# Kernel optimization log

Measured on AMD Instinct MI355X. Metric: run time of the kernel, lower is better.

Reference implementation:

```python
import jax, jax.numpy as jnp
import numpy as np

N = 100000
E = 1600000
IN_DIM = 64
HID = 64


def _glorot(key, shape):
    fan_in, fan_out = shape[0], shape[1]
    lim = np.sqrt(6.0 / (fan_in + fan_out))
    return jax.random.uniform(key, shape, jnp.float32, -lim, lim)


def setup_inputs() -> dict:
    key = jax.random.key(0)
    ks = jax.random.split(key, 14)
    x = jax.random.normal(ks[0], (N, IN_DIM), jnp.float32)
    edge_index = jax.random.randint(ks[1], (2, E), 0, N, jnp.int64)
    dims = [(IN_DIM, HID), (HID, HID), (HID, HID), (HID, 1)]
    inp = {"x": x, "edge_index": edge_index}
    for i, (di, do) in enumerate(dims, start=1):
        inp[f"Wself{i}"] = _glorot(ks[2 + 3 * (i - 1)], (di, do))
        inp[f"Wneigh{i}"] = _glorot(ks[3 + 3 * (i - 1)], (di, do))
        inp[f"b{i}"] = jnp.zeros((do,), jnp.float32)
    return inp


def _gn_block(h, src, dst, deg_inv, Wself, Wneigh, b, act):
    # gather -> scatter-add -> mean -> dense transform (GraphConv-style)
    msg = h[src]                                           # [E, d]
    agg = jax.ops.segment_sum(msg, dst, num_segments=N)    # [N, d]
    agg = agg * deg_inv                                    # mean aggregation
    out = h @ Wself + agg @ Wneigh + b
    return act(out)


def reference(x, edge_index, Wself1, Wneigh1, b1, Wself2, Wneigh2, b2,
              Wself3, Wneigh3, b3, Wself4, Wneigh4, b4):
    src, dst = edge_index[0], edge_index[1]
    deg = jax.ops.segment_sum(jnp.ones((E,), x.dtype), dst, num_segments=N)
    deg_inv = (1.0 / jnp.maximum(deg, 1.0))[:, None]       # [N, 1]
    relu = jax.nn.relu
    h = _gn_block(x, src, dst, deg_inv, Wself1, Wneigh1, b1, relu)
    h = _gn_block(h, src, dst, deg_inv, Wself2, Wneigh2, b2, relu)
    h = _gn_block(h, src, dst, deg_inv, Wself3, Wneigh3, b3, relu)
    h = _gn_block(h, src, dst, deg_inv, Wself4, Wneigh4, b4, lambda z: z)
    return jax.nn.sigmoid(h)                               # [N, 1]
```

## Files before the change

kernel.cpp:

```cpp
#include <hip/hip_runtime.h>
#include <hip/hip_bf16.h>
#include <math.h>


using bfrag = __attribute__((ext_vector_type(8))) short;
using ffrag = __attribute__((ext_vector_type(4))) float;

#define BKT_SHIFT 9
#define BKT_NODES (1 << BKT_SHIFT)

__device__ __forceinline__ int load_idx32(const int* __restrict__ ei32, int is64,
                                          long long pos) {
    return is64 ? ei32[2 * pos] : ei32[pos];
}

__device__ __forceinline__ unsigned short f2b_rne(float f) {
    union { float f; unsigned u; } c;
    c.f = f;
    unsigned r = c.u + 0x7FFFu + ((c.u >> 16) & 1u);
    return (unsigned short)(r >> 16);
}

__device__ __forceinline__ float b2f(unsigned short u) {
    union { unsigned u; float f; } c;
    c.u = ((unsigned)u) << 16;
    return c.f;
}

__global__ void bprep_init_kernel(
    const float* __restrict__ Ws1, const float* __restrict__ Wn1,
    const float* __restrict__ Ws2, const float* __restrict__ Wn2,
    const float* __restrict__ Ws3, const float* __restrict__ Wn3,
    unsigned short* __restrict__ bthi, unsigned short* __restrict__ btlo,
    const int* __restrict__ ei, int* __restrict__ bktc, int* __restrict__ flag) {
    if (blockIdx.x == 0) {
        bktc[threadIdx.x] = 0;
        if (threadIdx.x == 0) {
            int allz = 1;
            for (int i = 0; i < 32; ++i)
                if (ei[2 * i + 1] != 0) allz = 0;
            *flag = allz;
        }
    }
    int i = blockIdx.x * 256 + threadIdx.x;
    if (i >= 3 * 8192) return;
    int layer = i >> 13;
    int j = i & 8191;
    int n = j >> 7, k = j & 127;
    const float* Ws = layer == 0 ? Ws1 : (layer == 1 ? Ws2 : Ws3);
    const float* Wn = layer == 0 ? Wn1 : (layer == 1 ? Wn2 : Wn3);
    float v = (k < 64) ? Ws[k * 64 + n] : Wn[(k - 64) * 64 + n];
    unsigned short hi = f2b_rne(v);
    bthi[i] = hi;
    btlo[i] = f2b_rne(v - b2f(hi));
}

__global__ void split_x_kernel(const float4* __restrict__ in, ushort4* __restrict__ hi,
                               int n4) {
    int i = blockIdx.x * blockDim.x + threadIdx.x;
    if (i >= n4) return;
    float4 v = in[i];
    ushort4 h;
    h.x = f2b_rne(v.x); h.y = f2b_rne(v.y); h.z = f2b_rne(v.z); h.w = f2b_rne(v.w);
    hi[i] = h;
}

__global__ __launch_bounds__(256) void binA_kernel(
    const int* __restrict__ ei32, const int* __restrict__ flagp,
    int* __restrict__ bktCnt, unsigned* __restrict__ bins, int E, int nbkt,
    int cap, int chunksz) {
    __shared__ int cnt[256];
    __shared__ int base[256];
    int is64 = *flagp;
    int elo = blockIdx.x * chunksz;
    int ehi = min(E, elo + chunksz);
    if (elo >= E) return;
    for (int i = threadIdx.x; i < nbkt; i += 256) cnt[i] = 0;
    __syncthreads();
    for (int e = elo + (int)threadIdx.x; e < ehi; e += 256) {
        int dst = load_idx32(ei32, is64, (long long)E + e);
        atomicAdd(&cnt[dst >> BKT_SHIFT], 1);
    }
    __syncthreads();
    for (int i = threadIdx.x; i < nbkt; i += 256) {
        base[i] = atomicAdd(&bktCnt[i], cnt[i]);
        cnt[i] = 0;
    }
    __syncthreads();
    for (int e = elo + (int)threadIdx.x; e < ehi; e += 256) {
        int dst = load_idx32(ei32, is64, (long long)E + e);
        int src = load_idx32(ei32, is64, e);
        int b = dst >> BKT_SHIFT;
        int r = atomicAdd(&cnt[b], 1);
        bins[(size_t)b * cap + base[b] + r] =
            ((unsigned)(dst & (BKT_NODES - 1)) << 23) | (unsigned)src;
    }
}

__global__ __launch_bounds__(256) void bucketCSR_kernel(
    const int* __restrict__ bktCnt, const unsigned* __restrict__ bins,
    int* __restrict__ off, int* __restrict__ offe, int* __restrict__ col,
    float* __restrict__ dinv, int N, int cap) {
    __shared__ int deg[BKT_NODES];
    __shared__ int loc[BKT_NODES];
    __shared__ int ssum[256];
    int b = blockIdx.x;
    int lo = b << BKT_SHIFT;
    int n = min(BKT_NODES, N - lo);
    for (int i = threadIdx.x; i < BKT_NODES; i += 256) deg[i] = 0;
    __syncthreads();
    int cnt = bktCnt[b];
    const unsigned* bb = bins + (size_t)b * cap;
    for (int i = threadIdx.x; i < cnt; i += 256)
        atomicAdd(&deg[bb[i] >> 23], 1);
    __syncthreads();
    int t = threadIdx.x;
    int d0 = deg[2 * t], d1 = deg[2 * t + 1];
    int s = d0 + d1;
    ssum[t] = s;
    __syncthreads();
    for (int o = 1; o < 256; o <<= 1) {
        int v = (t >= o) ? ssum[t - o] : 0;
        __syncthreads();
        ssum[t] += v;
        __syncthreads();
    }
    int excl = ssum[t] - s;
    loc[2 * t] = excl;
    loc[2 * t + 1] = excl + d0;
    __syncthreads();
    int base = b * cap;
    for (int i = threadIdx.x; i < n; i += 256) {
        int d = deg[i];
        off[lo + i] = base + loc[i];
        offe[lo + i] = base + loc[i] + d;
        dinv[lo + i] = 1.0f / fmaxf((float)d, 1.0f);
    }
    __syncthreads();
    for (int i = threadIdx.x; i < cnt; i += 256) {
        unsigned p = bb[i];
        int pos = atomicAdd(&loc[p >> 23], 1);
        col[base + pos] = (int)(p & 0x7FFFFFu);
    }
}

#define AGG_STRIDE 72
__global__ __launch_bounds__(256) void layer_fused_kernel(
    const unsigned short* __restrict__ Hhi, const int* __restrict__ off,
    const int* __restrict__ offe, const int* __restrict__ col,
    const float* __restrict__ dinv,
    const unsigned short* __restrict__ Bthi, const unsigned short* __restrict__ Btlo,
    const float* __restrict__ b, unsigned short* __restrict__ Dhi, int N) {
    __shared__ unsigned short aggL[4 * 16 * AGG_STRIDE];
    int wave = threadIdx.x >> 6;
    int lane = threadIdx.x & 63;
    int g = lane >> 4;
    int t16 = lane & 15;
    int n0 = blockIdx.x * 64 + wave * 16;
    unsigned short* myAgg = aggL + wave * 16 * AGG_STRIDE;
    for (int i = 0; i < 16; ++i) {
        int n = n0 + i;
        if (n >= N) {
            if (g == 0) {
                ushort4 z = {0, 0, 0, 0};
                *(ushort4*)&myAgg[i * AGG_STRIDE + t16 * 4] = z;
            }
            continue;
        }
        int e = off[n], end = offe[n];
        float4 a0 = make_float4(0.f, 0.f, 0.f, 0.f);
        float4 a1 = make_float4(0.f, 0.f, 0.f, 0.f);
        float4 a2 = make_float4(0.f, 0.f, 0.f, 0.f);
        float4 a3 = make_float4(0.f, 0.f, 0.f, 0.f);
        for (; e + 16 <= end; e += 16) {
            int s0 = col[e + g];
            int s1 = col[e + 4 + g];
            int s2 = col[e + 8 + g];
            int s3 = col[e + 12 + g];
            ushort4 u0 = *(const ushort4*)&Hhi[(size_t)s0 * 64 + t16 * 4];
            ushort4 u1 = *(const ushort4*)&Hhi[(size_t)s1 * 64 + t16 * 4];
            ushort4 u2 = *(const ushort4*)&Hhi[(size_t)s2 * 64 + t16 * 4];
            ushort4 u3 = *(const ushort4*)&Hhi[(size_t)s3 * 64 + t16 * 4];
            a0.x += b2f(u0.x); a0.y += b2f(u0.y); a0.z += b2f(u0.z); a0.w += b2f(u0.w);
            a1.x += b2f(u1.x); a1.y += b2f(u1.y); a1.z += b2f(u1.z); a1.w += b2f(u1.w);
            a2.x += b2f(u2.x); a2.y += b2f(u2.y); a2.z += b2f(u2.z); a2.w += b2f(u2.w);
            a3.x += b2f(u3.x); a3.y += b2f(u3.y); a3.z += b2f(u3.z); a3.w += b2f(u3.w);
        }
        for (; e + 8 <= end; e += 8) {
            int s0 = col[e + g];
            int s1 = col[e + 4 + g];
            ushort4 u0 = *(const ushort4*)&Hhi[(size_t)s0 * 64 + t16 * 4];
            ushort4 u1 = *(const ushort4*)&Hhi[(size_t)s1 * 64 + t16 * 4];
            a0.x += b2f(u0.x); a0.y += b2f(u0.y); a0.z += b2f(u0.z); a0.w += b2f(u0.w);
            a1.x += b2f(u1.x); a1.y += b2f(u1.y); a1.z += b2f(u1.z); a1.w += b2f(u1.w);
        }
        for (; e < end; e += 4) {
            if (e + g < end) {
                int s0 = col[e + g];
                ushort4 u0 = *(const ushort4*)&Hhi[(size_t)s0 * 64 + t16 * 4];
                a2.x += b2f(u0.x); a2.y += b2f(u0.y); a2.z += b2f(u0.z); a2.w += b2f(u0.w);
            }
        }
        float4 acc;
        acc.x = (a0.x + a1.x) + (a2.x + a3.x);
        acc.y = (a0.y + a1.y) + (a2.y + a3.y);
        acc.z = (a0.z + a1.z) + (a2.z + a3.z);
        acc.w = (a0.w + a1.w) + (a2.w + a3.w);
#pragma unroll
        for (int msk = 16; msk <= 32; msk <<= 1) {
            acc.x += __shfl_xor(acc.x, msk, 64);
            acc.y += __shfl_xor(acc.y, msk, 64);
            acc.z += __shfl_xor(acc.z, msk, 64);
            acc.w += __shfl_xor(acc.w, msk, 64);
        }
        if (g == 0) {
            float di = dinv[n];
            ushort4 h;
            h.x = f2b_rne(acc.x * di);
            h.y = f2b_rne(acc.y * di);
            h.z = f2b_rne(acc.z * di);
            h.w = f2b_rne(acc.w * di);
            *(ushort4*)&myAgg[i * AGG_STRIDE + t16 * 4] = h;
        }
    }
    int m = t16, quad = g;
    int nr = n0 + m;
    if (nr > N - 1) nr = N - 1;
    const unsigned short* hrow = Hhi + (size_t)nr * 64 + quad * 8;
    bfrag ah[4];
    ah[0] = *(const bfrag*)(hrow);
    ah[1] = *(const bfrag*)(hrow + 32);
    ah[2] = *(const bfrag*)&myAgg[m * AGG_STRIDE + quad * 8];
    ah[3] = *(const bfrag*)&myAgg[m * AGG_STRIDE + 32 + quad * 8];
#pragma unroll
    for (int t = 0; t < 4; ++t) {
        float bl = b[t * 16 + m];
        ffrag acc = {bl, bl, bl, bl};
#pragma unroll
        for (int c = 0; c < 4; ++c) {
            bfrag bh = *(const bfrag*)(Bthi + (size_t)(t * 16 + m) * 128 + c * 32 + quad * 8);
            bfrag bw = *(const bfrag*)(Btlo + (size_t)(t * 16 + m) * 128 + c * 32 + quad * 8);
            acc = __builtin_amdgcn_mfma_f32_16x16x32_bf16(ah[c], bh, acc, 0, 0, 0);
            acc = __builtin_amdgcn_mfma_f32_16x16x32_bf16(ah[c], bw, acc, 0, 0, 0);
        }
#pragma unroll
        for (int r = 0; r < 4; ++r) {
            int node = n0 + quad * 4 + r;
            if (node < N)
                Dhi[(size_t)node * 64 + t * 16 + m] = f2b_rne(fmaxf(acc[r], 0.f));
        }
    }
}

__global__ __launch_bounds__(256) void layer_fused_last_kernel(
    const unsigned short* __restrict__ Hhi, const int* __restrict__ off,
    const int* __restrict__ offe, const int* __restrict__ col,
    const float* __restrict__ dinv,
    const unsigned short* __restrict__ Bthi, const unsigned short* __restrict__ Btlo,
    const float* __restrict__ b, const float* __restrict__ Ws4,
    const float* __restrict__ Wn4, float* __restrict__ sbuf,
    float* __restrict__ gbuf, int N) {
    __shared__ unsigned short aggL[4 * 16 * AGG_STRIDE];
    int wave = threadIdx.x >> 6;
    int lane = threadIdx.x & 63;
    int g = lane >> 4;
    int t16 = lane & 15;
    int n0 = blockIdx.x * 64 + wave * 16;
    unsigned short* myAgg = aggL + wave * 16 * AGG_STRIDE;
    for (int i = 0; i < 16; ++i) {
        int n = n0 + i;
        if (n >= N) {
            if (g == 0) {
                ushort4 z = {0, 0, 0, 0};
                *(ushort4*)&myAgg[i * AGG_STRIDE + t16 * 4] = z;
            }
            continue;
        }
        int e = off[n], end = offe[n];
        float4 a0 = make_float4(0.f, 0.f, 0.f, 0.f);
        float4 a1 = make_float4(0.f, 0.f, 0.f, 0.f);
        float4 a2 = make_float4(0.f, 0.f, 0.f, 0.f);
        float4 a3 = make_float4(0.f, 0.f, 0.f, 0.f);
        for (; e + 16 <= end; e += 16) {
            int s0 = col[e + g];
            int s1 = col[e + 4 + g];
            int s2 = col[e + 8 + g];
            int s3 = col[e + 12 + g];
            ushort4 u0 = *(const ushort4*)&Hhi[(size_t)s0 * 64 + t16 * 4];
            ushort4 u1 = *(const ushort4*)&Hhi[(size_t)s1 * 64 + t16 * 4];
            ushort4 u2 = *(const ushort4*)&Hhi[(size_t)s2 * 64 + t16 * 4];
            ushort4 u3 = *(const ushort4*)&Hhi[(size_t)s3 * 64 + t16 * 4];
            a0.x += b2f(u0.x); a0.y += b2f(u0.y); a0.z += b2f(u0.z); a0.w += b2f(u0.w);
            a1.x += b2f(u1.x); a1.y += b2f(u1.y); a1.z += b2f(u1.z); a1.w += b2f(u1.w);
            a2.x += b2f(u2.x); a2.y += b2f(u2.y); a2.z += b2f(u2.z); a2.w += b2f(u2.w);
            a3.x += b2f(u3.x); a3.y += b2f(u3.y); a3.z += b2f(u3.z); a3.w += b2f(u3.w);
        }
        for (; e + 8 <= end; e += 8) {
            int s0 = col[e + g];
            int s1 = col[e + 4 + g];
            ushort4 u0 = *(const ushort4*)&Hhi[(size_t)s0 * 64 + t16 * 4];
            ushort4 u1 = *(const ushort4*)&Hhi[(size_t)s1 * 64 + t16 * 4];
            a0.x += b2f(u0.x); a0.y += b2f(u0.y); a0.z += b2f(u0.z); a0.w += b2f(u0.w);
            a1.x += b2f(u1.x); a1.y += b2f(u1.y); a1.z += b2f(u1.z); a1.w += b2f(u1.w);
        }
        for (; e < end; e += 4) {
            if (e + g < end) {
                int s0 = col[e + g];
                ushort4 u0 = *(const ushort4*)&Hhi[(size_t)s0 * 64 + t16 * 4];
                a2.x += b2f(u0.x); a2.y += b2f(u0.y); a2.z += b2f(u0.z); a2.w += b2f(u0.w);
            }
        }
        float4 acc;
        acc.x = (a0.x + a1.x) + (a2.x + a3.x);
        acc.y = (a0.y + a1.y) + (a2.y + a3.y);
        acc.z = (a0.z + a1.z) + (a2.z + a3.z);
        acc.w = (a0.w + a1.w) + (a2.w + a3.w);
#pragma unroll
        for (int msk = 16; msk <= 32; msk <<= 1) {
            acc.x += __shfl_xor(acc.x, msk, 64);
            acc.y += __shfl_xor(acc.y, msk, 64);
            acc.z += __shfl_xor(acc.z, msk, 64);
            acc.w += __shfl_xor(acc.w, msk, 64);
        }
        if (g == 0) {
            float di = dinv[n];
            ushort4 h;
            h.x = f2b_rne(acc.x * di);
            h.y = f2b_rne(acc.y * di);
            h.z = f2b_rne(acc.z * di);
            h.w = f2b_rne(acc.w * di);
            *(ushort4*)&myAgg[i * AGG_STRIDE + t16 * 4] = h;
        }
    }
    int m = t16, quad = g;
    int nr = n0 + m;
    if (nr > N - 1) nr = N - 1;
    const unsigned short* hrow = Hhi + (size_t)nr * 64 + quad * 8;
    bfrag ah[4];
    ah[0] = *(const bfrag*)(hrow);
    ah[1] = *(const bfrag*)(hrow + 32);
    ah[2] = *(const bfrag*)&myAgg[m * AGG_STRIDE + quad * 8];
    ah[3] = *(const bfrag*)&myAgg[m * AGG_STRIDE + 32 + quad * 8];
    ffrag accs[4];
#pragma unroll
    for (int t = 0; t < 4; ++t) {
        float bl = b[t * 16 + m];
        ffrag acc = {bl, bl, bl, bl};
#pragma unroll
        for (int c = 0; c < 4; ++c) {
            bfrag bh = *(const bfrag*)(Bthi + (size_t)(t * 16 + m) * 128 + c * 32 + quad * 8);
            bfrag bw = *(const bfrag*)(Btlo + (size_t)(t * 16 + m) * 128 + c * 32 + quad * 8);
            acc = __builtin_amdgcn_mfma_f32_16x16x32_bf16(ah[c], bh, acc, 0, 0, 0);
            acc = __builtin_amdgcn_mfma_f32_16x16x32_bf16(ah[c], bw, acc, 0, 0, 0);
        }
        accs[t] = acc;
    }
    float w4s[4], w4n[4];
#pragma unroll
    for (int t = 0; t < 4; ++t) {
        w4s[t] = Ws4[t * 16 + m];
        w4n[t] = Wn4[t * 16 + m];
    }
#pragma unroll
    for (int r = 0; r < 4; ++r) {
        float ps = 0.f, pg = 0.f;
#pragma unroll
        for (int t = 0; t < 4; ++t) {
            float v = fmaxf(accs[t][r], 0.f);
            ps = fmaf(v, w4s[t], ps);
            pg = fmaf(v, w4n[t], pg);
        }
#pragma unroll
        for (int mask = 1; mask <= 8; mask <<= 1) {
            ps += __shfl_xor(ps, mask, 64);
            pg += __shfl_xor(pg, mask, 64);
        }
        int node = n0 + quad * 4 + r;
        if (m == 0 && node < N) {
            sbuf[node] = ps;
            gbuf[node] = pg;
        }
    }
}

__global__ void final_kernel(const float* __restrict__ s, const float* __restrict__ dinv,
                             const float* __restrict__ g, const int* __restrict__ off,
                             const int* __restrict__ offe, const int* __restrict__ col,
                             const float* __restrict__ b4, float* __restrict__ out, int N) {
    int n = blockIdx.x * blockDim.x + threadIdx.x;
    if (n >= N) return;
    float a = 0.f;
    int e = off[n], end = offe[n];
    for (; e < end; ++e) a += g[col[e]];
    float z = s[n] + dinv[n] * a + b4[0];
    out[n] = 1.0f / (1.0f + expf(-z));
}

static inline int cdiv(long long a, long long b) { return (int)((a + b - 1) / b); }

extern "C" void kernel_launch(void* const* d_in, const int* in_sizes, int n_in,
                              void* d_out, int out_size, void* d_ws, size_t ws_size,
                              hipStream_t stream) {
    const float* x   = (const float*)d_in[0];
    const int*   ei  = (const int*)d_in[1];
    const float* Ws1 = (const float*)d_in[2];
    const float* Wn1 = (const float*)d_in[3];
    const float* b1  = (const float*)d_in[4];
    const float* Ws2 = (const float*)d_in[5];
    const float* Wn2 = (const float*)d_in[6];
    const float* b2  = (const float*)d_in[7];
    const float* Ws3 = (const float*)d_in[8];
    const float* Wn3 = (const float*)d_in[9];
    const float* b3  = (const float*)d_in[10];
    const float* Ws4 = (const float*)d_in[11];
    const float* Wn4 = (const float*)d_in[12];
    const float* b4  = (const float*)d_in[13];
    float* out = (float*)d_out;

    const int N = in_sizes[0] / 64;
    const int E = in_sizes[1] / 2;

    const int nbkt = cdiv(N, BKT_NODES);
    const int cap  = E / nbkt + E / nbkt / 8 + 64;

    unsigned* bins = (unsigned*)d_ws;
    int* col = (int*)(bins + (size_t)nbkt * cap);
    unsigned short* HhiA = (unsigned short*)(col + (size_t)nbkt * cap);
    unsigned short* HhiB = HhiA + (size_t)N * 64;
    unsigned short* Bth  = HhiB + (size_t)N * 64;
    unsigned short* Btl  = Bth + 3 * 8192;
    float* dinv = (float*)(Btl + 3 * 8192);
    float* sbuf = dinv + N;
    float* gbuf = sbuf + N;
    int*   off  = (int*)(gbuf + N);
    int*   offe = off + N;
    int*   bktc = offe + N;
    int*   flag = bktc + 256;

    const int BT = 256;
    const int gridN  = cdiv(N, BT);
    const int gridL  = cdiv(N, 64);
    const int binBlocks = 512;
    const int chunksz = cdiv(E, binBlocks);

    bprep_init_kernel<<<96, BT, 0, stream>>>(Ws1, Wn1, Ws2, Wn2, Ws3, Wn3,
                                             Bth, Btl, ei, bktc, flag);
    split_x_kernel<<<cdiv((long long)N * 16, BT), BT, 0, stream>>>(
        (const float4*)x, (ushort4*)HhiA, N * 16);

    binA_kernel<<<binBlocks, BT, 0, stream>>>(ei, flag, bktc, bins, E, nbkt, cap, chunksz);
    bucketCSR_kernel<<<nbkt, BT, 0, stream>>>(bktc, bins, off, offe, col, dinv, N, cap);

    layer_fused_kernel<<<gridL, BT, 0, stream>>>(HhiA, off, offe, col, dinv,
                                                 Bth, Btl, b1, HhiB, N);
    layer_fused_kernel<<<gridL, BT, 0, stream>>>(HhiB, off, offe, col, dinv,
                                                 Bth + 8192, Btl + 8192, b2, HhiA, N);
    layer_fused_last_kernel<<<gridL, BT, 0, stream>>>(HhiA, off, offe, col, dinv,
                                                      Bth + 16384, Btl + 16384, b3,
                                                      Ws4, Wn4, sbuf, gbuf, N);

    final_kernel<<<gridN, BT, 0, stream>>>(sbuf, dinv, gbuf, off, offe, col, b4, out, N);
}
```

Measured before the change: 417.3 us.

## Split layer blocks to 16 nodes with waves sharing gather and output columns

```diff
diff --git a/kernel.cpp b/kernel.cpp
--- a/kernel.cpp
+++ b/kernel.cpp
@@ -8,6 +8,7 @@
 
 #define BKT_SHIFT 9
 #define BKT_NODES (1 << BKT_SHIFT)
+#define AGG_STRIDE 72
 
 __device__ __forceinline__ int load_idx32(const int* __restrict__ ei32, int is64,
                                           long long pos) {
@@ -144,85 +145,94 @@
     }
 }
 
-#define AGG_STRIDE 72
+__device__ __forceinline__ void gather_node(
+    const unsigned short* __restrict__ Hhi, const int* __restrict__ off,
+    const int* __restrict__ offe, const int* __restrict__ col,
+    const float* __restrict__ dinv, unsigned short* __restrict__ aggRow,
+    int n, int N, int g, int t16) {
+    if (n >= N) {
+        if (g == 0) {
+            ushort4 z = {0, 0, 0, 0};
+            *(ushort4*)&aggRow[t16 * 4] = z;
+        }
+        return;
+    }
+    int e = off[n], end = offe[n];
+    float4 a0 = make_float4(0.f, 0.f, 0.f, 0.f);
+    float4 a1 = make_float4(0.f, 0.f, 0.f, 0.f);
+    float4 a2 = make_float4(0.f, 0.f, 0.f, 0.f);
+    float4 a3 = make_float4(0.f, 0.f, 0.f, 0.f);
+    for (; e + 16 <= end; e += 16) {
+        int s0 = col[e + g];
+        int s1 = col[e + 4 + g];
+        int s2 = col[e + 8 + g];
+        int s3 = col[e + 12 + g];
+        ushort4 u0 = *(const ushort4*)&Hhi[(size_t)s0 * 64 + t16 * 4];
+        ushort4 u1 = *(const ushort4*)&Hhi[(size_t)s1 * 64 + t16 * 4];
+        ushort4 u2 = *(const ushort4*)&Hhi[(size_t)s2 * 64 + t16 * 4];
+        ushort4 u3 = *(const ushort4*)&Hhi[(size_t)s3 * 64 + t16 * 4];
+        a0.x += b2f(u0.x); a0.y += b2f(u0.y); a0.z += b2f(u0.z); a0.w += b2f(u0.w);
+        a1.x += b2f(u1.x); a1.y += b2f(u1.y); a1.z += b2f(u1.z); a1.w += b2f(u1.w);
+        a2.x += b2f(u2.x); a2.y += b2f(u2.y); a2.z += b2f(u2.z); a2.w += b2f(u2.w);
+        a3.x += b2f(u3.x); a3.y += b2f(u3.y); a3.z += b2f(u3.z); a3.w += b2f(u3.w);
+    }
+    for (; e + 8 <= end; e += 8) {
+        int s0 = col[e + g];
+        int s1 = col[e + 4 + g];
+        ushort4 u0 = *(const ushort4*)&Hhi[(size_t)s0 * 64 + t16 * 4];
+        ushort4 u1 = *(const ushort4*)&Hhi[(size_t)s1 * 64 + t16 * 4];
+        a0.x += b2f(u0.x); a0.y += b2f(u0.y); a0.z += b2f(u0.z); a0.w += b2f(u0.w);
+        a1.x += b2f(u1.x); a1.y += b2f(u1.y); a1.z += b2f(u1.z); a1.w += b2f(u1.w);
+    }
+    for (; e < end; e += 4) {
+        if (e + g < end) {
+            int s0 = col[e + g];
+            ushort4 u0 = *(const ushort4*)&Hhi[(size_t)s0 * 64 + t16 * 4];
+            a2.x += b2f(u0.x); a2.y += b2f(u0.y); a2.z += b2f(u0.z); a2.w += b2f(u0.w);
+        }
+    }
+    float4 acc;
+    acc.x = (a0.x + a1.x) + (a2.x + a3.x);
+    acc.y = (a0.y + a1.y) + (a2.y + a3.y);
+    acc.z = (a0.z + a1.z) + (a2.z + a3.z);
+    acc.w = (a0.w + a1.w) + (a2.w + a3.w);
+#pragma unroll
+    for (int msk = 16; msk <= 32; msk <<= 1) {
+        acc.x += __shfl_xor(acc.x, msk, 64);
+        acc.y += __shfl_xor(acc.y, msk, 64);
+        acc.z += __shfl_xor(acc.z, msk, 64);
+        acc.w += __shfl_xor(acc.w, msk, 64);
+    }
+    if (g == 0) {
+        float di = dinv[n];
+        ushort4 h;
+        h.x = f2b_rne(acc.x * di);
+        h.y = f2b_rne(acc.y * di);
+        h.z = f2b_rne(acc.z * di);
+        h.w = f2b_rne(acc.w * di);
+        *(ushort4*)&aggRow[t16 * 4] = h;
+    }
+}
+
 __global__ __launch_bounds__(256) void layer_fused_kernel(
     const unsigned short* __restrict__ Hhi, const int* __restrict__ off,
     const int* __restrict__ offe, const int* __restrict__ col,
     const float* __restrict__ dinv,
     const unsigned short* __restrict__ Bthi, const unsigned short* __restrict__ Btlo,
     const float* __restrict__ b, unsigned short* __restrict__ Dhi, int N) {
-    __shared__ unsigned short aggL[4 * 16 * AGG_STRIDE];
+    __shared__ unsigned short aggL[16 * AGG_STRIDE];
     int wave = threadIdx.x >> 6;
     int lane = threadIdx.x & 63;
     int g = lane >> 4;
     int t16 = lane & 15;
-    int n0 = blockIdx.x * 64 + wave * 16;
-    unsigned short* myAgg = aggL + wave * 16 * AGG_STRIDE;
-    for (int i = 0; i < 16; ++i) {
-        int n = n0 + i;
-        if (n >= N) {
-            if (g == 0) {
-                ushort4 z = {0, 0, 0, 0};
-                *(ushort4*)&myAgg[i * AGG_STRIDE + t16 * 4] = z;
-            }
-            continue;
-        }
-        int e = off[n], end = offe[n];
-        float4 a0 = make_float4(0.f, 0.f, 0.f, 0.f);
-        float4 a1 = make_float4(0.f, 0.f, 0.f, 0.f);
-        float4 a2 = make_float4(0.f, 0.f, 0.f, 0.f);
-        float4 a3 = make_float4(0.f, 0.f, 0.f, 0.f);
-        for (; e + 16 <= end; e += 16) {
-            int s0 = col[e + g];
-            int s1 = col[e + 4 + g];
-            int s2 = col[e + 8 + g];
-            int s3 = col[e + 12 + g];
-            ushort4 u0 = *(const ushort4*)&Hhi[(size_t)s0 * 64 + t16 * 4];
-            ushort4 u1 = *(const ushort4*)&Hhi[(size_t)s1 * 64 + t16 * 4];
-            ushort4 u2 = *(const ushort4*)&Hhi[(size_t)s2 * 64 + t16 * 4];
-            ushort4 u3 = *(const ushort4*)&Hhi[(size_t)s3 * 64 + t16 * 4];
-            a0.x += b2f(u0.x); a0.y += b2f(u0.y); a0.z += b2f(u0.z); a0.w += b2f(u0.w);
-            a1.x += b2f(u1.x); a1.y += b2f(u1.y); a1.z += b2f(u1.z); a1.w += b2f(u1.w);
-            a2.x += b2f(u2.x); a2.y += b2f(u2.y); a2.z += b2f(u2.z); a2.w += b2f(u2.w);
-            a3.x += b2f(u3.x); a3.y += b2f(u3.y); a3.z += b2f(u3.z); a3.w += b2f(u3.w);
-        }
-        for (; e + 8 <= end; e += 8) {
-            int s0 = col[e + g];
-            int s1 = col[e + 4 + g];
-            ushort4 u0 = *(const ushort4*)&Hhi[(size_t)s0 * 64 + t16 * 4];
-            ushort4 u1 = *(const ushort4*)&Hhi[(size_t)s1 * 64 + t16 * 4];
-            a0.x += b2f(u0.x); a0.y += b2f(u0.y); a0.z += b2f(u0.z); a0.w += b2f(u0.w);
-            a1.x += b2f(u1.x); a1.y += b2f(u1.y); a1.z += b2f(u1.z); a1.w += b2f(u1.w);
-        }
-        for (; e < end; e += 4) {
-            if (e + g < end) {
-                int s0 = col[e + g];
-                ushort4 u0 = *(const ushort4*)&Hhi[(size_t)s0 * 64 + t16 * 4];
-                a2.x += b2f(u0.x); a2.y += b2f(u0.y); a2.z += b2f(u0.z); a2.w += b2f(u0.w);
-            }
-        }
-        float4 acc;
-        acc.x = (a0.x + a1.x) + (a2.x + a3.x);
-        acc.y = (a0.y + a1.y) + (a2.y + a3.y);
-        acc.z = (a0.z + a1.z) + (a2.z + a3.z);
-        acc.w = (a0.w + a1.w) + (a2.w + a3.w);
-#pragma unroll
-        for (int msk = 16; msk <= 32; msk <<= 1) {
-            acc.x += __shfl_xor(acc.x, msk, 64);
-            acc.y += __shfl_xor(acc.y, msk, 64);
-            acc.z += __shfl_xor(acc.z, msk, 64);
-            acc.w += __shfl_xor(acc.w, msk, 64);
-        }
-        if (g == 0) {
-            float di = dinv[n];
-            ushort4 h;
-            h.x = f2b_rne(acc.x * di);
-            h.y = f2b_rne(acc.y * di);
-            h.z = f2b_rne(acc.z * di);
-            h.w = f2b_rne(acc.w * di);
-            *(ushort4*)&myAgg[i * AGG_STRIDE + t16 * 4] = h;
-        }
-    }
+    int n0 = blockIdx.x * 16;
+#pragma unroll
+    for (int i = 0; i < 4; ++i) {
+        int li = wave * 4 + i;
+        gather_node(Hhi, off, offe, col, dinv, aggL + li * AGG_STRIDE,
+                    n0 + li, N, g, t16);
+    }
+    __syncthreads();
     int m = t16, quad = g;
     int nr = n0 + m;
     if (nr > N - 1) nr = N - 1;
@@ -230,25 +240,23 @@
     bfrag ah[4];
     ah[0] = *(const bfrag*)(hrow);
     ah[1] = *(const bfrag*)(hrow + 32);
-    ah[2] = *(const bfrag*)&myAgg[m * AGG_STRIDE + quad * 8];
-    ah[3] = *(const bfrag*)&myAgg[m * AGG_STRIDE + 32 + quad * 8];
-#pragma unroll
-    for (int t = 0; t < 4; ++t) {
-        float bl = b[t * 16 + m];
-        ffrag acc = {bl, bl, bl, bl};
-#pragma unroll
-        for (int c = 0; c < 4; ++c) {
-            bfrag bh = *(const bfrag*)(Bthi + (size_t)(t * 16 + m) * 128 + c * 32 + quad * 8);
-            bfrag bw = *(const bfrag*)(Btlo + (size_t)(t * 16 + m) * 128 + c * 32 + quad * 8);
-            acc = __builtin_amdgcn_mfma_f32_16x16x32_bf16(ah[c], bh, acc, 0, 0, 0);
-            acc = __builtin_amdgcn_mfma_f32_16x16x32_bf16(ah[c], bw, acc, 0, 0, 0);
-        }
-#pragma unroll
-        for (int r = 0; r < 4; ++r) {
-            int node = n0 + quad * 4 + r;
-            if (node < N)
-                Dhi[(size_t)node * 64 + t * 16 + m] = f2b_rne(fmaxf(acc[r], 0.f));
-        }
+    ah[2] = *(const bfrag*)&aggL[m * AGG_STRIDE + quad * 8];
+    ah[3] = *(const bfrag*)&aggL[m * AGG_STRIDE + 32 + quad * 8];
+    int oc = wave * 16 + m;
+    float bl = b[oc];
+    ffrag acc = {bl, bl, bl, bl};
+#pragma unroll
+    for (int c = 0; c < 4; ++c) {
+        bfrag bh = *(const bfrag*)(Bthi + (size_t)oc * 128 + c * 32 + quad * 8);
+        bfrag bw = *(const bfrag*)(Btlo + (size_t)oc * 128 + c * 32 + quad * 8);
+        acc = __builtin_amdgcn_mfma_f32_16x16x32_bf16(ah[c], bh, acc, 0, 0, 0);
+        acc = __builtin_amdgcn_mfma_f32_16x16x32_bf16(ah[c], bw, acc, 0, 0, 0);
+    }
+#pragma unroll
+    for (int r = 0; r < 4; ++r) {
+        int node = n0 + quad * 4 + r;
+        if (node < N)
+            Dhi[(size_t)node * 64 + oc] = f2b_rne(fmaxf(acc[r], 0.f));
     }
 }
 
@@ -260,78 +268,21 @@
     const float* __restrict__ b, const float* __restrict__ Ws4,
     const float* __restrict__ Wn4, float* __restrict__ sbuf,
     float* __restrict__ gbuf, int N) {
-    __shared__ unsigned short aggL[4 * 16 * AGG_STRIDE];
+    __shared__ unsigned short aggL[16 * AGG_STRIDE];
+    __shared__ float sPart[4][16];
+    __shared__ float gPart[4][16];
     int wave = threadIdx.x >> 6;
     int lane = threadIdx.x & 63;
     int g = lane >> 4;
     int t16 = lane & 15;
-    int n0 = blockIdx.x * 64 + wave * 16;
-    unsigned short* myAgg = aggL + wave * 16 * AGG_STRIDE;
-    for (int i = 0; i < 16; ++i) {
-        int n = n0 + i;
-        if (n >= N) {
-            if (g == 0) {
-                ushort4 z = {0, 0, 0, 0};
-                *(ushort4*)&myAgg[i * AGG_STRIDE + t16 * 4] = z;
-            }
-            continue;
-        }
-        int e = off[n], end = offe[n];
-        float4 a0 = make_float4(0.f, 0.f, 0.f, 0.f);
-        float4 a1 = make_float4(0.f, 0.f, 0.f, 0.f);
-        float4 a2 = make_float4(0.f, 0.f, 0.f, 0.f);
-        float4 a3 = make_float4(0.f, 0.f, 0.f, 0.f);
-        for (; e + 16 <= end; e += 16) {
-            int s0 = col[e + g];
-            int s1 = col[e + 4 + g];
-            int s2 = col[e + 8 + g];
-            int s3 = col[e + 12 + g];
-            ushort4 u0 = *(const ushort4*)&Hhi[(size_t)s0 * 64 + t16 * 4];
-            ushort4 u1 = *(const ushort4*)&Hhi[(size_t)s1 * 64 + t16 * 4];
-            ushort4 u2 = *(const ushort4*)&Hhi[(size_t)s2 * 64 + t16 * 4];
-            ushort4 u3 = *(const ushort4*)&Hhi[(size_t)s3 * 64 + t16 * 4];
-            a0.x += b2f(u0.x); a0.y += b2f(u0.y); a0.z += b2f(u0.z); a0.w += b2f(u0.w);
-            a1.x += b2f(u1.x); a1.y += b2f(u1.y); a1.z += b2f(u1.z); a1.w += b2f(u1.w);
-            a2.x += b2f(u2.x); a2.y += b2f(u2.y); a2.z += b2f(u2.z); a2.w += b2f(u2.w);
-            a3.x += b2f(u3.x); a3.y += b2f(u3.y); a3.z += b2f(u3.z); a3.w += b2f(u3.w);
-        }
-        for (; e + 8 <= end; e += 8) {
-            int s0 = col[e + g];
-            int s1 = col[e + 4 + g];
-            ushort4 u0 = *(const ushort4*)&Hhi[(size_t)s0 * 64 + t16 * 4];
-            ushort4 u1 = *(const ushort4*)&Hhi[(size_t)s1 * 64 + t16 * 4];
-            a0.x += b2f(u0.x); a0.y += b2f(u0.y); a0.z += b2f(u0.z); a0.w += b2f(u0.w);
-            a1.x += b2f(u1.x); a1.y += b2f(u1.y); a1.z += b2f(u1.z); a1.w += b2f(u1.w);
-        }
-        for (; e < end; e += 4) {
-            if (e + g < end) {
-                int s0 = col[e + g];
-                ushort4 u0 = *(const ushort4*)&Hhi[(size_t)s0 * 64 + t16 * 4];
-                a2.x += b2f(u0.x); a2.y += b2f(u0.y); a2.z += b2f(u0.z); a2.w += b2f(u0.w);
-            }
-        }
-        float4 acc;
-        acc.x = (a0.x + a1.x) + (a2.x + a3.x);
-        acc.y = (a0.y + a1.y) + (a2.y + a3.y);
-        acc.z = (a0.z + a1.z) + (a2.z + a3.z);
-        acc.w = (a0.w + a1.w) + (a2.w + a3.w);
-#pragma unroll
-        for (int msk = 16; msk <= 32; msk <<= 1) {
-            acc.x += __shfl_xor(acc.x, msk, 64);
-            acc.y += __shfl_xor(acc.y, msk, 64);
-            acc.z += __shfl_xor(acc.z, msk, 64);
-            acc.w += __shfl_xor(acc.w, msk, 64);
-        }
-        if (g == 0) {
-            float di = dinv[n];
-            ushort4 h;
-            h.x = f2b_rne(acc.x * di);
-            h.y = f2b_rne(acc.y * di);
-            h.z = f2b_rne(acc.z * di);
-            h.w = f2b_rne(acc.w * di);
-            *(ushort4*)&myAgg[i * AGG_STRIDE + t16 * 4] = h;
-        }
-    }
+    int n0 = blockIdx.x * 16;
+#pragma unroll
+    for (int i = 0; i < 4; ++i) {
+        int li = wave * 4 + i;
+        gather_node(Hhi, off, offe, col, dinv, aggL + li * AGG_STRIDE,
+                    n0 + li, N, g, t16);
+    }
+    __syncthreads();
     int m = t16, quad = g;
     int nr = n0 + m;
     if (nr > N - 1) nr = N - 1;
@@ -339,46 +290,44 @@
     bfrag ah[4];
     ah[0] = *(const bfrag*)(hrow);
     ah[1] = *(const bfrag*)(hrow + 32);
-    ah[2] = *(const bfrag*)&myAgg[m * AGG_STRIDE + quad * 8];
-    ah[3] = *(const bfrag*)&myAgg[m * AGG_STRIDE + 32 + quad * 8];
-    ffrag accs[4];
-#pragma unroll
-    for (int t = 0; t < 4; ++t) {
-        float bl = b[t * 16 + m];
-        ffrag acc = {bl, bl, bl, bl};
-#pragma unroll
-        for (int c = 0; c < 4; ++c) {
-            bfrag bh = *(const bfrag*)(Bthi + (size_t)(t * 16 + m) * 128 + c * 32 + quad * 8);
-            bfrag bw = *(const bfrag*)(Btlo + (size_t)(t * 16 + m) * 128 + c * 32 + quad * 8);
-            acc = __builtin_amdgcn_mfma_f32_16x16x32_bf16(ah[c], bh, acc, 0, 0, 0);
-            acc = __builtin_amdgcn_mfma_f32_16x16x32_bf16(ah[c], bw, acc, 0, 0, 0);
-        }
-        accs[t] = acc;
-    }
-    float w4s[4], w4n[4];
-#pragma unroll
-    for (int t = 0; t < 4; ++t) {
-        w4s[t] = Ws4[t * 16 + m];
-        w4n[t] = Wn4[t * 16 + m];
-    }
+    ah[2] = *(const bfrag*)&aggL[m * AGG_STRIDE + quad * 8];
+    ah[3] = *(const bfrag*)&aggL[m * AGG_STRIDE + 32 + quad * 8];
+    int oc = wave * 16 + m;
+    float bl = b[oc];
+    ffrag acc = {bl, bl, bl, bl};
+#pragma unroll
+    for (int c = 0; c < 4; ++c) {
+        bfrag bh = *(const bfrag*)(Bthi + (size_t)oc * 128 + c * 32 + quad * 8);
+        bfrag bw = *(const bfrag*)(Btlo + (size_t)oc * 128 + c * 32 + quad * 8);
+        acc = __builtin_amdgcn_mfma_f32_16x16x32_bf16(ah[c], bh, acc, 0, 0, 0);
+        acc = __builtin_amdgcn_mfma_f32_16x16x32_bf16(ah[c], bw, acc, 0, 0, 0);
+    }
+    float w4s = Ws4[oc], w4n = Wn4[oc];
 #pragma unroll
     for (int r = 0; r < 4; ++r) {
-        float ps = 0.f, pg = 0.f;
-#pragma unroll
-        for (int t = 0; t < 4; ++t) {
-            float v = fmaxf(accs[t][r], 0.f);
-            ps = fmaf(v, w4s[t], ps);
-            pg = fmaf(v, w4n[t], pg);
-        }
+        float v = fmaxf(acc[r], 0.f);
+        float ps = v * w4s;
+        float pg = v * w4n;
 #pragma unroll
         for (int mask = 1; mask <= 8; mask <<= 1) {
             ps += __shfl_xor(ps, mask, 64);
             pg += __shfl_xor(pg, mask, 64);
         }
-        int node = n0 + quad * 4 + r;
-        if (m == 0 && node < N) {
-            sbuf[node] = ps;
-            gbuf[node] = pg;
+        if (m == 0) {
+            sPart[wave][quad * 4 + r] = ps;
+            gPart[wave][quad * 4 + r] = pg;
+        }
+    }
+    __syncthreads();
+    if (threadIdx.x < 16) {
+        int node = n0 + threadIdx.x;
+        if (node < N) {
+            float s = sPart[0][threadIdx.x] + sPart[1][threadIdx.x] +
+                      sPart[2][threadIdx.x] + sPart[3][threadIdx.x];
+            float gg = gPart[0][threadIdx.x] + gPart[1][threadIdx.x] +
+                       gPart[2][threadIdx.x] + gPart[3][threadIdx.x];
+            sbuf[node] = s;
+            gbuf[node] = gg;
         }
     }
 }
@@ -439,7 +388,7 @@
 
     const int BT = 256;
     const int gridN  = cdiv(N, BT);
-    const int gridL  = cdiv(N, 64);
+    const int gridL  = cdiv(N, 16);
     const int binBlocks = 512;
     const int chunksz = cdiv(E, binBlocks);
 
```

After: 404.6 us. -3.0%, faster.
